# Optimization experiments

Hardware: AMD Instinct MI355X
Metric: run time of the kernel (lower is better)

The kernel has to match this reference:

```python
import jax, jax.numpy as jnp
import numpy as np

N_CHANNELS = 1024
N_HEADS = 16
BLOCK_SIZE = 2048
BATCH = 4
SEQ = 2048


def setup_inputs() -> dict:
    key = jax.random.key(0)
    k_x, k_wqkv, k_wproj = jax.random.split(key, 3)
    x = jax.random.normal(k_x, (BATCH, SEQ, N_CHANNELS), dtype=jnp.float32)
    # torch nn.Linear: y = x @ W.T + b, W shape [out, in], init normal(std=0.02)
    W_qkv = jax.random.normal(k_wqkv, (3 * N_CHANNELS, N_CHANNELS), dtype=jnp.float32) * 0.02
    b_qkv = jnp.zeros((3 * N_CHANNELS,), dtype=jnp.float32)
    W_proj = jax.random.normal(k_wproj, (N_CHANNELS, N_CHANNELS), dtype=jnp.float32) * 0.02
    b_proj = jnp.zeros((N_CHANNELS,), dtype=jnp.float32)
    return {"x": x, "W_qkv": W_qkv, "b_qkv": b_qkv, "W_proj": W_proj, "b_proj": b_proj}


def reference(x, W_qkv, b_qkv, W_proj, b_proj):
    bs, n, n_channels = x.shape
    n_heads = N_HEADS
    head_dim = n_channels // n_heads
    scale = head_dim ** (-0.5)

    qkv = x @ W_qkv.T + b_qkv                              # [b, n, 3C]
    qkv = qkv.reshape(bs, n, 3, n_heads, head_dim)
    q, k, v = qkv[:, :, 0], qkv[:, :, 1], qkv[:, :, 2]     # [b, n, h, d]

    logits = jnp.einsum('bthc,bshc->bhts', q, k) * scale   # [b, h, t, s]
    # causal mask: log(tril(ones)) = 0 below diagonal, -inf above
    causal = jnp.tril(jnp.ones((n, n), dtype=bool))
    logits = jnp.where(causal[None, None], logits, -jnp.inf)
    attn = jax.nn.softmax(logits, axis=-1)

    output = jnp.einsum('bhts,bshc->bthc', attn, v)        # [b, t, h, d]
    output = output.reshape(bs, n, n_channels)
    output = output @ W_proj.T + b_proj
    return output
```

## Files before the change

kernel.cpp:

```cpp
#include <hip/hip_runtime.h>
#include <hip/hip_bf16.h>
#include <stdint.h>

#define BATCH 4
#define SEQ   2048
#define NC    1024
#define NH    16
#define HD    64
#define NT    16

typedef __bf16 bf16x8 __attribute__((ext_vector_type(8)));
typedef __bf16 bf16x4 __attribute__((ext_vector_type(4)));
typedef float  f32x4  __attribute__((ext_vector_type(4)));

#define DEV __device__ __forceinline__

DEV unsigned short f2bf(float f) {
    union { float f; unsigned u; } v; v.f = f;
    unsigned r = (v.u + 0x7fffu + ((v.u >> 16) & 1u)) >> 16;
    return (unsigned short)r;
}

DEV float fast_exp2(float x) {
#if __has_builtin(__builtin_amdgcn_exp2f)
    return __builtin_amdgcn_exp2f(x);
#else
    return exp2f(x);
#endif
}

#define GLDS16(gsrc, ldst)                                                           \
    __builtin_amdgcn_global_load_lds(                                                \
        (const __attribute__((address_space(1))) unsigned int*)(gsrc),               \
        (__attribute__((address_space(3))) unsigned int*)(ldst), 16, 0, 0)

__global__ void cvt_kernel(const float* __restrict__ in, unsigned short* __restrict__ out, int n4) {
    int i = blockIdx.x * 256 + threadIdx.x;
    if (i >= n4) return;
    float4 v = reinterpret_cast<const float4*>(in)[i];
    ushort4 o;
    o.x = f2bf(v.x); o.y = f2bf(v.y); o.z = f2bf(v.z); o.w = f2bf(v.w);
    reinterpret_cast<ushort4*>(out)[i] = o;
}

template <bool BF16_OUT>
__global__ __launch_bounds__(256, 2) void gemm_bt_kernel(
    const unsigned short* __restrict__ A,
    const unsigned short* __restrict__ W,
    const float* __restrict__ bias,
    void* __restrict__ Cout,
    int M, int N, int K, int scale_n, float scale)
{
    __shared__ __align__(16) char Alds[128 * 128];
    __shared__ __align__(16) char Blds[128 * 128];

    const int tid = threadIdx.x;
    const int w = tid >> 6, l = tid & 63, g = l >> 4, lr = l & 15;
    const int nt = N >> 7;
    const int cpx = gridDim.x >> 3;
    const int bid = (blockIdx.x & 7) * cpx + (blockIdx.x >> 3);
    const int mtile = bid / nt, ntile = bid % nt;
    const int m0 = mtile << 7, n0 = ntile << 7;
    const int wr = (w >> 1) << 6, wc = (w & 1) << 6;

    f32x4 acc[4][4] = {};

    for (int kt = 0; kt < K; kt += 64) {
        if (kt) __syncthreads();
#pragma unroll
        for (int i = 0; i < 4; ++i) {
            const int issue = (i << 2) + w;
            const int row = (issue << 3) + (l >> 3);
            const int chunk = (l & 7) ^ (row & 7);
            GLDS16((const char*)(A + (size_t)(m0 + row) * K + kt) + (chunk << 4),
                   Alds + (issue << 10));
        }
#pragma unroll
        for (int i = 0; i < 4; ++i) {
            const int issue = (i << 2) + w;
            const int row = (issue << 3) + (l >> 3);
            const int chunk = (l & 7) ^ (row & 7);
            GLDS16((const char*)(W + (size_t)(n0 + row) * K + kt) + (chunk << 4),
                   Blds + (issue << 10));
        }
        __syncthreads();

#pragma unroll
        for (int kb = 0; kb < 2; ++kb) {
            bf16x8 af[4], bfr[4];
#pragma unroll
            for (int mf = 0; mf < 4; ++mf) {
                const int row = wr + (mf << 4) + lr;
                const int chunk = ((kb << 2) + g) ^ (row & 7);
                af[mf] = *reinterpret_cast<const bf16x8*>(Alds + row * 128 + (chunk << 4));
            }
#pragma unroll
            for (int nf = 0; nf < 4; ++nf) {
                const int row = wc + (nf << 4) + lr;
                const int chunk = ((kb << 2) + g) ^ (row & 7);
                bfr[nf] = *reinterpret_cast<const bf16x8*>(Blds + row * 128 + (chunk << 4));
            }
#pragma unroll
            for (int mf = 0; mf < 4; ++mf)
#pragma unroll
                for (int nf = 0; nf < 4; ++nf)
                    acc[mf][nf] = __builtin_amdgcn_mfma_f32_16x16x32_bf16(
                        af[mf], bfr[nf], acc[mf][nf], 0, 0, 0);
        }
    }

#pragma unroll
    for (int mf = 0; mf < 4; ++mf) {
#pragma unroll
        for (int nf = 0; nf < 4; ++nf) {
            const int n = n0 + wc + (nf << 4) + lr;
            const float bscale = (n < scale_n) ? scale : 1.0f;
            const float bv = bias[n];
#pragma unroll
            for (int r = 0; r < 4; ++r) {
                const int m = m0 + wr + (mf << 4) + (g << 2) + r;
                float v2 = (acc[mf][nf][r] + bv) * bscale;
                if (BF16_OUT)
                    ((unsigned short*)Cout)[(size_t)m * N + n] = f2bf(v2);
                else
                    ((float*)Cout)[(size_t)m * N + n] = v2;
            }
        }
    }
}

__global__ __launch_bounds__(256, 2) void attn_kernel(
    const unsigned short* __restrict__ qkv,
    unsigned short* __restrict__ ctx)
{
    __shared__ __align__(16) char Klds[2][8192];
    __shared__ __align__(16) char Vt[2][64 * 144];
    __shared__ __align__(16) char Pl[4][32 * 144];

    const int tid = threadIdx.x;
    const int w = tid >> 6, l = tid & 63, g = l >> 4, lr = l & 15;
    const int bid = blockIdx.x;
    const int qt = NT - 1 - (bid >> 6);
    const int h = (bid >> 2) & 15, b = bid & 3;
    const unsigned short* base = qkv + (size_t)b * SEQ * 3072 + h * 64;
    char* Pw = Pl[w];

    const int vkey0 = (tid >> 5) << 3;
    const int vd0   = (tid & 31) << 1;
    const unsigned short* vbase = base + 2048 + (size_t)vkey0 * 3072 + vd0;

    const int q0 = (qt << 7) + (w << 5);
    const int ntiles = (qt + 1) << 1;

    bf16x8 qfr[2][2];
#pragma unroll
    for (int qi = 0; qi < 2; ++qi)
#pragma unroll
        for (int kb = 0; kb < 2; ++kb)
            qfr[qi][kb] = *reinterpret_cast<const bf16x8*>(
                base + (size_t)(q0 + (qi << 4) + lr) * 3072 + (kb << 5) + (g << 3));

    f32x4 acc[2][4] = {};
    float mrun[2] = {-INFINITY, -INFINITY};
    float lrun[2] = {0.f, 0.f};

    uint32_t vreg[8];

#pragma unroll
    for (int i = 0; i < 8; ++i)
        vreg[i] = *reinterpret_cast<const uint32_t*>(vbase + (size_t)i * 3072);
#pragma unroll
    for (int i = 0; i < 2; ++i) {
        const int issue = (i << 2) + w;
        const int row = (issue << 3) + (l >> 3);
        const int chunk = (l & 7) ^ (row & 7);
        GLDS16((const char*)(base + 1024 + (size_t)row * 3072) + (chunk << 4),
               Klds[0] + (issue << 10));
    }
    {
        uint4 a, bq;
        a.x = (vreg[0] & 0xffffu) | (vreg[1] << 16);
        a.y = (vreg[2] & 0xffffu) | (vreg[3] << 16);
        a.z = (vreg[4] & 0xffffu) | (vreg[5] << 16);
        a.w = (vreg[6] & 0xffffu) | (vreg[7] << 16);
        bq.x = (vreg[0] >> 16) | (vreg[1] & 0xffff0000u);
        bq.y = (vreg[2] >> 16) | (vreg[3] & 0xffff0000u);
        bq.z = (vreg[4] >> 16) | (vreg[5] & 0xffff0000u);
        bq.w = (vreg[6] >> 16) | (vreg[7] & 0xffff0000u);
        *reinterpret_cast<uint4*>(Vt[0] + vd0 * 144 + vkey0 * 2) = a;
        *reinterpret_cast<uint4*>(Vt[0] + (vd0 + 1) * 144 + vkey0 * 2) = bq;
    }
    __syncthreads();

    for (int t = 0; t < ntiles; ++t) {
        const int cur = t & 1;
        const int kv0 = t << 6;
        const bool pf_ = (t + 1 < ntiles);

        if (pf_) {
            const int kv1 = kv0 + 64;
#pragma unroll
            for (int i = 0; i < 8; ++i)
                vreg[i] = *reinterpret_cast<const uint32_t*>(
                    vbase + (size_t)(kv1 + i) * 3072);
#pragma unroll
            for (int i = 0; i < 2; ++i) {
                const int issue = (i << 2) + w;
                const int row = (issue << 3) + (l >> 3);
                const int chunk = (l & 7) ^ (row & 7);
                GLDS16((const char*)(base + 1024 + (size_t)(kv1 + row) * 3072) + (chunk << 4),
                       Klds[cur ^ 1] + (issue << 10));
            }
        }

        if (kv0 <= q0 + 31) {
            f32x4 st[4][2] = {};
#pragma unroll
            for (int kb = 0; kb < 2; ++kb) {
                bf16x8 kfr[4];
#pragma unroll
                for (int kf = 0; kf < 4; ++kf) {
                    const int row = (kf << 4) + lr;
                    const int chunk = ((kb << 2) + g) ^ (row & 7);
                    kfr[kf] = *reinterpret_cast<const bf16x8*>(
                        Klds[cur] + row * 128 + (chunk << 4));
                }
#pragma unroll
                for (int kf = 0; kf < 4; ++kf)
#pragma unroll
                    for (int qi = 0; qi < 2; ++qi)
                        st[kf][qi] = __builtin_amdgcn_mfma_f32_16x16x32_bf16(
                            kfr[kf], qfr[qi][kb], st[kf][qi], 0, 0, 0);
            }
#pragma unroll
            for (int qi = 0; qi < 2; ++qi) {
                if (kv0 + 63 > q0 + (qi << 4)) {
                    const int qg = q0 + (qi << 4) + lr;
#pragma unroll
                    for (int kf = 0; kf < 4; ++kf)
#pragma unroll
                        for (int r = 0; r < 4; ++r) {
                            const int key = kv0 + (kf << 4) + (g << 2) + r;
                            if (key > qg) st[kf][qi][r] = -INFINITY;
                        }
                }
                float mt = -INFINITY;
#pragma unroll
                for (int kf = 0; kf < 4; ++kf)
#pragma unroll
                    for (int r = 0; r < 4; ++r) mt = fmaxf(mt, st[kf][qi][r]);
                mt = fmaxf(mt, __shfl_xor(mt, 16));
                mt = fmaxf(mt, __shfl_xor(mt, 32));
                if (__any(mt > mrun[qi] + 8.0f)) {
                    const float mnew = fmaxf(mrun[qi], mt);
                    const float corr = fast_exp2(mrun[qi] - mnew);
                    mrun[qi] = mnew;
                    lrun[qi] *= corr;
#pragma unroll
                    for (int df = 0; df < 4; ++df)
#pragma unroll
                        for (int r = 0; r < 4; ++r) acc[qi][df][r] *= corr;
                }
                float rs = 0.f;
#pragma unroll
                for (int kf = 0; kf < 4; ++kf) {
                    float p0 = fast_exp2(st[kf][qi][0] - mrun[qi]);
                    float p1 = fast_exp2(st[kf][qi][1] - mrun[qi]);
                    float p2 = fast_exp2(st[kf][qi][2] - mrun[qi]);
                    float p3 = fast_exp2(st[kf][qi][3] - mrun[qi]);
                    rs += (p0 + p1) + (p2 + p3);
                    bf16x4 pv = {(__bf16)p0, (__bf16)p1, (__bf16)p2, (__bf16)p3};
                    *reinterpret_cast<bf16x4*>(
                        Pw + (qi * 16 + lr) * 144 + (((kf << 4) + (g << 2)) << 1)) = pv;
                }
                rs += __shfl_xor(rs, 16);
                rs += __shfl_xor(rs, 32);
                lrun[qi] += rs;
            }
#pragma unroll
            for (int kb = 0; kb < 2; ++kb) {
                bf16x8 pfv[2], vf[4];
#pragma unroll
                for (int qi = 0; qi < 2; ++qi)
                    pfv[qi] = *reinterpret_cast<const bf16x8*>(
                        Pw + (qi * 16 + lr) * 144 + (((kb << 5) + (g << 3)) << 1));
#pragma unroll
                for (int df = 0; df < 4; ++df)
                    vf[df] = *reinterpret_cast<const bf16x8*>(
                        Vt[cur] + ((df << 4) + lr) * 144 + (((kb << 5) + (g << 3)) << 1));
#pragma unroll
                for (int qi = 0; qi < 2; ++qi)
#pragma unroll
                    for (int df = 0; df < 4; ++df)
                        acc[qi][df] = __builtin_amdgcn_mfma_f32_16x16x32_bf16(
                            vf[df], pfv[qi], acc[qi][df], 0, 0, 0);
            }
        }

        if (pf_) {
            uint4 a, bq;
            a.x = (vreg[0] & 0xffffu) | (vreg[1] << 16);
            a.y = (vreg[2] & 0xffffu) | (vreg[3] << 16);
            a.z = (vreg[4] & 0xffffu) | (vreg[5] << 16);
            a.w = (vreg[6] & 0xffffu) | (vreg[7] << 16);
            bq.x = (vreg[0] >> 16) | (vreg[1] & 0xffff0000u);
            bq.y = (vreg[2] >> 16) | (vreg[3] & 0xffff0000u);
            bq.z = (vreg[4] >> 16) | (vreg[5] & 0xffff0000u);
            bq.w = (vreg[6] >> 16) | (vreg[7] & 0xffff0000u);
            char* vt = Vt[cur ^ 1];
            *reinterpret_cast<uint4*>(vt + vd0 * 144 + vkey0 * 2) = a;
            *reinterpret_cast<uint4*>(vt + (vd0 + 1) * 144 + vkey0 * 2) = bq;
            __syncthreads();
        }
    }

#pragma unroll
    for (int qi = 0; qi < 2; ++qi) {
        const float li = 1.0f / lrun[qi];
        const int q = q0 + (qi << 4) + lr;
        unsigned short* op = ctx + (size_t)(b * SEQ + q) * NC + h * HD;
#pragma unroll
        for (int df = 0; df < 4; ++df)
#pragma unroll
            for (int r = 0; r < 4; ++r)
                op[(df << 4) + (g << 2) + r] = f2bf(acc[qi][df][r] * li);
    }
}

extern "C" void kernel_launch(void* const* d_in, const int* in_sizes, int n_in,
                              void* d_out, int out_size, void* d_ws, size_t ws_size,
                              hipStream_t stream) {
    const float* x     = (const float*)d_in[0];
    const float* Wqkv  = (const float*)d_in[1];
    const float* bqkv  = (const float*)d_in[2];
    const float* Wproj = (const float*)d_in[3];
    const float* bproj = (const float*)d_in[4];
    float* out = (float*)d_out;

    const int M = BATCH * SEQ;
    unsigned short* ws = (unsigned short*)d_ws;
    unsigned short* xb     = ws;
    unsigned short* wqkvb  = xb + (size_t)M * NC;
    unsigned short* wprojb = wqkvb + (size_t)3 * NC * NC;
    unsigned short* qkvb   = wprojb + (size_t)NC * NC;
    unsigned short* ctxb   = qkvb + (size_t)M * 3 * NC;

    {
        int n4 = M * NC / 4;
        cvt_kernel<<<(n4 + 255) / 256, 256, 0, stream>>>(x, xb, n4);
    }
    {
        int n4 = 3 * NC * NC / 4;
        cvt_kernel<<<(n4 + 255) / 256, 256, 0, stream>>>(Wqkv, wqkvb, n4);
    }
    {
        int n4 = NC * NC / 4;
        cvt_kernel<<<(n4 + 255) / 256, 256, 0, stream>>>(Wproj, wprojb, n4);
    }

    gemm_bt_kernel<true><<<(M / 128) * (3 * NC / 128), 256, 0, stream>>>(
        xb, wqkvb, bqkv, qkvb, M, 3 * NC, NC, NC, 0.18033688011112042f);

    attn_kernel<<<NT * NH * BATCH, 256, 0, stream>>>(qkvb, ctxb);

    gemm_bt_kernel<false><<<(M / 128) * (NC / 128), 256, 0, stream>>>(
        ctxb, wprojb, bproj, out, M, NC, NC, 0, 1.0f);
}
```

Before: 164.1 us.

## Use 32x32 MFMA in attention, keep P in registers via permlane32 swap

Rewrites the attention inner loop to use 32x32x16 bf16 MFMA tiles, so each lane owns one query row and the softmax reductions need one cross-half shuffle instead of two. The probability tile no longer goes through an LDS staging buffer: it is packed to bf16 in registers and rearranged with permlane32_swap into the B-operand layout for the PV MFMA. It also skips the second 32-key half of a tile when it lies fully above the causal diagonal, and raises the launch bound to 4 blocks per CU, which removes the P LDS buffer and its round trip. The risk is register pressure from the 16-wide accumulators at the higher occupancy target, plus a fallback shuffle path if the builtin is missing.

Result: faster. 158.8 us (-3.2%).

```diff
diff --git a/kernel.cpp b/kernel.cpp
--- a/kernel.cpp
+++ b/kernel.cpp
@@ -10,8 +10,9 @@
 #define NT    16
 
 typedef __bf16 bf16x8 __attribute__((ext_vector_type(8)));
-typedef __bf16 bf16x4 __attribute__((ext_vector_type(4)));
+typedef __bf16 bf16x2 __attribute__((ext_vector_type(2)));
 typedef float  f32x4  __attribute__((ext_vector_type(4)));
+typedef float  f32x16 __attribute__((ext_vector_type(16)));
 
 #define DEV __device__ __forceinline__
 
@@ -26,6 +27,20 @@
     return __builtin_amdgcn_exp2f(x);
 #else
     return exp2f(x);
+#endif
+}
+
+DEV void plane32_swap(uint32_t& a, uint32_t& b) {
+#if __has_builtin(__builtin_amdgcn_permlane32_swap)
+    auto r = __builtin_amdgcn_permlane32_swap(a, b, false, false);
+    a = (uint32_t)r[0];
+    b = (uint32_t)r[1];
+#else
+    uint32_t sa = __shfl_xor(a, 32), sb = __shfl_xor(b, 32);
+    const bool hi = ((threadIdx.x & 63) >= 32);
+    uint32_t na = hi ? sb : a;
+    uint32_t nb = hi ? b : sa;
+    a = na; b = nb;
 #endif
 }
 
@@ -129,40 +144,36 @@
     }
 }
 
-__global__ __launch_bounds__(256, 2) void attn_kernel(
+__global__ __launch_bounds__(256, 4) void attn_kernel(
     const unsigned short* __restrict__ qkv,
     unsigned short* __restrict__ ctx)
 {
     __shared__ __align__(16) char Klds[2][8192];
     __shared__ __align__(16) char Vt[2][64 * 144];
-    __shared__ __align__(16) char Pl[4][32 * 144];
 
     const int tid = threadIdx.x;
-    const int w = tid >> 6, l = tid & 63, g = l >> 4, lr = l & 15;
+    const int w = tid >> 6, l = tid & 63, hi = l >> 5, lq = l & 31;
     const int bid = blockIdx.x;
     const int qt = NT - 1 - (bid >> 6);
     const int h = (bid >> 2) & 15, b = bid & 3;
     const unsigned short* base = qkv + (size_t)b * SEQ * 3072 + h * 64;
-    char* Pw = Pl[w];
 
     const int vkey0 = (tid >> 5) << 3;
     const int vd0   = (tid & 31) << 1;
     const unsigned short* vbase = base + 2048 + (size_t)vkey0 * 3072 + vd0;
 
     const int q0 = (qt << 7) + (w << 5);
+    const int q = q0 + lq;
     const int ntiles = (qt + 1) << 1;
 
-    bf16x8 qfr[2][2];
-#pragma unroll
-    for (int qi = 0; qi < 2; ++qi)
-#pragma unroll
-        for (int kb = 0; kb < 2; ++kb)
-            qfr[qi][kb] = *reinterpret_cast<const bf16x8*>(
-                base + (size_t)(q0 + (qi << 4) + lr) * 3072 + (kb << 5) + (g << 3));
-
-    f32x4 acc[2][4] = {};
-    float mrun[2] = {-INFINITY, -INFINITY};
-    float lrun[2] = {0.f, 0.f};
+    bf16x8 qfr[4];
+#pragma unroll
+    for (int ds = 0; ds < 4; ++ds)
+        qfr[ds] = *reinterpret_cast<const bf16x8*>(
+            base + (size_t)q * 3072 + (ds << 4) + (hi << 3));
+
+    f32x16 acc0 = {}, acc1 = {};
+    float mrun = -INFINITY, lrun = 0.f;
 
     uint32_t vreg[8];
 
@@ -214,86 +225,110 @@
         }
 
         if (kv0 <= q0 + 31) {
-            f32x4 st[4][2] = {};
-#pragma unroll
-            for (int kb = 0; kb < 2; ++kb) {
-                bf16x8 kfr[4];
-#pragma unroll
-                for (int kf = 0; kf < 4; ++kf) {
-                    const int row = (kf << 4) + lr;
-                    const int chunk = ((kb << 2) + g) ^ (row & 7);
-                    kfr[kf] = *reinterpret_cast<const bf16x8*>(
-                        Klds[cur] + row * 128 + (chunk << 4));
+            const bool do1 = (kv0 + 32 <= q0 + 31);
+
+            f32x16 st0 = {}, st1 = {};
+#pragma unroll
+            for (int ds = 0; ds < 4; ++ds) {
+                const int chunk = (((ds << 1) + hi) ^ (lq & 7)) << 4;
+                bf16x8 k0 = *reinterpret_cast<const bf16x8*>(
+                    Klds[cur] + lq * 128 + chunk);
+                st0 = __builtin_amdgcn_mfma_f32_32x32x16_bf16(k0, qfr[ds], st0, 0, 0, 0);
+            }
+            if (do1) {
+#pragma unroll
+                for (int ds = 0; ds < 4; ++ds) {
+                    const int chunk = (((ds << 1) + hi) ^ (lq & 7)) << 4;
+                    bf16x8 k1 = *reinterpret_cast<const bf16x8*>(
+                        Klds[cur] + (lq + 32) * 128 + chunk);
+                    st1 = __builtin_amdgcn_mfma_f32_32x32x16_bf16(k1, qfr[ds], st1, 0, 0, 0);
                 }
-#pragma unroll
-                for (int kf = 0; kf < 4; ++kf)
-#pragma unroll
-                    for (int qi = 0; qi < 2; ++qi)
-                        st[kf][qi] = __builtin_amdgcn_mfma_f32_16x16x32_bf16(
-                            kfr[kf], qfr[qi][kb], st[kf][qi], 0, 0, 0);
-            }
-#pragma unroll
-            for (int qi = 0; qi < 2; ++qi) {
-                if (kv0 + 63 > q0 + (qi << 4)) {
-                    const int qg = q0 + (qi << 4) + lr;
-#pragma unroll
-                    for (int kf = 0; kf < 4; ++kf)
-#pragma unroll
-                        for (int r = 0; r < 4; ++r) {
-                            const int key = kv0 + (kf << 4) + (g << 2) + r;
-                            if (key > qg) st[kf][qi][r] = -INFINITY;
-                        }
+            }
+
+            if (kv0 + 31 > q0) {
+#pragma unroll
+                for (int r = 0; r < 16; ++r) {
+                    const int key = kv0 + ((r & 3) + ((r >> 2) << 3) + (hi << 2));
+                    if (key > q) st0[r] = -INFINITY;
                 }
-                float mt = -INFINITY;
-#pragma unroll
-                for (int kf = 0; kf < 4; ++kf)
-#pragma unroll
-                    for (int r = 0; r < 4; ++r) mt = fmaxf(mt, st[kf][qi][r]);
-                mt = fmaxf(mt, __shfl_xor(mt, 16));
-                mt = fmaxf(mt, __shfl_xor(mt, 32));
-                if (__any(mt > mrun[qi] + 8.0f)) {
-                    const float mnew = fmaxf(mrun[qi], mt);
-                    const float corr = fast_exp2(mrun[qi] - mnew);
-                    mrun[qi] = mnew;
-                    lrun[qi] *= corr;
-#pragma unroll
-                    for (int df = 0; df < 4; ++df)
-#pragma unroll
-                        for (int r = 0; r < 4; ++r) acc[qi][df][r] *= corr;
+            }
+            if (do1 && kv0 + 63 > q0) {
+#pragma unroll
+                for (int r = 0; r < 16; ++r) {
+                    const int key = kv0 + 32 + ((r & 3) + ((r >> 2) << 3) + (hi << 2));
+                    if (key > q) st1[r] = -INFINITY;
                 }
-                float rs = 0.f;
-#pragma unroll
-                for (int kf = 0; kf < 4; ++kf) {
-                    float p0 = fast_exp2(st[kf][qi][0] - mrun[qi]);
-                    float p1 = fast_exp2(st[kf][qi][1] - mrun[qi]);
-                    float p2 = fast_exp2(st[kf][qi][2] - mrun[qi]);
-                    float p3 = fast_exp2(st[kf][qi][3] - mrun[qi]);
-                    rs += (p0 + p1) + (p2 + p3);
-                    bf16x4 pv = {(__bf16)p0, (__bf16)p1, (__bf16)p2, (__bf16)p3};
-                    *reinterpret_cast<bf16x4*>(
-                        Pw + (qi * 16 + lr) * 144 + (((kf << 4) + (g << 2)) << 1)) = pv;
+            }
+
+            float mt = st0[0];
+#pragma unroll
+            for (int r = 1; r < 16; ++r) mt = fmaxf(mt, st0[r]);
+            if (do1) {
+#pragma unroll
+                for (int r = 0; r < 16; ++r) mt = fmaxf(mt, st1[r]);
+            }
+            mt = fmaxf(mt, __shfl_xor(mt, 32));
+            if (__any(mt > mrun + 8.0f)) {
+                const float mnew = fmaxf(mrun, mt);
+                const float corr = fast_exp2(mrun - mnew);
+                mrun = mnew;
+                lrun *= corr;
+#pragma unroll
+                for (int r = 0; r < 16; ++r) { acc0[r] *= corr; acc1[r] *= corr; }
+            }
+            float rs = 0.f;
+#pragma unroll
+            for (int r = 0; r < 16; ++r) { st0[r] = fast_exp2(st0[r] - mrun); rs += st0[r]; }
+            if (do1) {
+#pragma unroll
+                for (int r = 0; r < 16; ++r) { st1[r] = fast_exp2(st1[r] - mrun); rs += st1[r]; }
+            }
+            rs += __shfl_xor(rs, 32);
+            lrun += rs;
+
+            uint32_t pk0[8], pk1[8];
+#pragma unroll
+            for (int s = 0; s < 4; ++s)
+#pragma unroll
+                for (int c = 0; c < 2; ++c) {
+                    bf16x2 t0 = {(__bf16)st0[(s << 2) + (c << 1)],
+                                 (__bf16)st0[(s << 2) + (c << 1) + 1]};
+                    pk0[(s << 1) + c] = __builtin_bit_cast(uint32_t, t0);
                 }
-                rs += __shfl_xor(rs, 16);
-                rs += __shfl_xor(rs, 32);
-                lrun[qi] += rs;
-            }
-#pragma unroll
-            for (int kb = 0; kb < 2; ++kb) {
-                bf16x8 pfv[2], vf[4];
-#pragma unroll
-                for (int qi = 0; qi < 2; ++qi)
-                    pfv[qi] = *reinterpret_cast<const bf16x8*>(
-                        Pw + (qi * 16 + lr) * 144 + (((kb << 5) + (g << 3)) << 1));
-#pragma unroll
-                for (int df = 0; df < 4; ++df)
-                    vf[df] = *reinterpret_cast<const bf16x8*>(
-                        Vt[cur] + ((df << 4) + lr) * 144 + (((kb << 5) + (g << 3)) << 1));
-#pragma unroll
-                for (int qi = 0; qi < 2; ++qi)
-#pragma unroll
-                    for (int df = 0; df < 4; ++df)
-                        acc[qi][df] = __builtin_amdgcn_mfma_f32_16x16x32_bf16(
-                            vf[df], pfv[qi], acc[qi][df], 0, 0, 0);
+            if (do1) {
+#pragma unroll
+                for (int s = 0; s < 4; ++s)
+#pragma unroll
+                    for (int c = 0; c < 2; ++c) {
+                        bf16x2 t1 = {(__bf16)st1[(s << 2) + (c << 1)],
+                                     (__bf16)st1[(s << 2) + (c << 1) + 1]};
+                        pk1[(s << 1) + c] = __builtin_bit_cast(uint32_t, t1);
+                    }
+            }
+
+            const int nkt = do1 ? 4 : 2;
+#pragma unroll
+            for (int kt = 0; kt < 4; ++kt) {
+                if (kt >= nkt) break;
+                const int s0 = (kt & 1) << 1;
+                uint32_t x0, x1, y0, y1;
+                if (kt < 2) {
+                    x0 = pk0[(s0 << 1) + 0]; x1 = pk0[(s0 << 1) + 1];
+                    y0 = pk0[(s0 << 1) + 2]; y1 = pk0[(s0 << 1) + 3];
+                } else {
+                    x0 = pk1[(s0 << 1) + 0]; x1 = pk1[(s0 << 1) + 1];
+                    y0 = pk1[(s0 << 1) + 2]; y1 = pk1[(s0 << 1) + 3];
+                }
+                plane32_swap(x0, y0);
+                plane32_swap(x1, y1);
+                union { uint32_t u[4]; bf16x8 v; } pf;
+                pf.u[0] = x0; pf.u[1] = x1; pf.u[2] = y0; pf.u[3] = y1;
+
+                const char* vrow = Vt[cur] + ((kt << 4) + (hi << 3)) * 2;
+                bf16x8 vf0 = *reinterpret_cast<const bf16x8*>(vrow + lq * 144);
+                bf16x8 vf1 = *reinterpret_cast<const bf16x8*>(vrow + (lq + 32) * 144);
+                acc0 = __builtin_amdgcn_mfma_f32_32x32x16_bf16(vf0, pf.v, acc0, 0, 0, 0);
+                acc1 = __builtin_amdgcn_mfma_f32_32x32x16_bf16(vf1, pf.v, acc1, 0, 0, 0);
             }
         }
 
@@ -314,16 +349,15 @@
         }
     }
 
-#pragma unroll
-    for (int qi = 0; qi < 2; ++qi) {
-        const float li = 1.0f / lrun[qi];
-        const int q = q0 + (qi << 4) + lr;
+    {
+        const float li = 1.0f / lrun;
         unsigned short* op = ctx + (size_t)(b * SEQ + q) * NC + h * HD;
 #pragma unroll
-        for (int df = 0; df < 4; ++df)
-#pragma unroll
-            for (int r = 0; r < 4; ++r)
-                op[(df << 4) + (g << 2) + r] = f2bf(acc[qi][df][r] * li);
+        for (int r = 0; r < 16; ++r) {
+            const int d = (r & 3) + ((r >> 2) << 3) + (hi << 2);
+            op[d] = f2bf(acc0[r] * li);
+            op[d + 32] = f2bf(acc1[r] * li);
+        }
     }
 }
 
```
